# Kernel tuning notes

Hardware: AMD Instinct MI355X
Metric: run time of the kernel (lower is better)

The kernel has to match this reference:

```python
import jax, jax.numpy as jnp
import numpy as np

N = 40000      # nodes
E = 640000     # edges (avg degree 16)
IN = 128
H = 128
OUT = 64


def setup_inputs() -> dict:
    key = jax.random.key(0)
    ks = jax.random.split(key, 10)
    s_in = 1.0 / np.sqrt(IN)
    s_h = 1.0 / np.sqrt(H)
    return {
        "x": jax.random.normal(ks[0], (N, IN), jnp.float32),
        "edge_index": jax.random.randint(ks[1], (2, E), 0, N, dtype=jnp.int64),
        "W1l": jax.random.normal(ks[2], (IN, H), jnp.float32) * s_in,
        "W1r": jax.random.normal(ks[3], (IN, H), jnp.float32) * s_in,
        "b1": jnp.zeros((H,), jnp.float32),
        "W2l": jax.random.normal(ks[4], (H, H), jnp.float32) * s_h,
        "W2r": jax.random.normal(ks[5], (H, H), jnp.float32) * s_h,
        "b2": jnp.zeros((H,), jnp.float32),
        "Wout": jax.random.normal(ks[6], (H, OUT), jnp.float32) * s_h,
        "bout": jnp.zeros((OUT,), jnp.float32),
    }


def _sage_conv(x, src, dst, Wl, Wr, b):
    # mean aggregation of source features onto destination nodes
    msg = x[src]                                   # [E, d] gather
    agg = jax.ops.segment_sum(msg, dst, num_segments=N)       # [N, d]
    deg = jax.ops.segment_sum(jnp.ones((src.shape[0],), x.dtype), dst,
                              num_segments=N)                  # [N]
    agg = agg / jnp.maximum(deg, 1.0)[:, None]
    # PyG SAGEConv: lin_l(aggregated neighbors) + lin_r(root); bias on lin_l
    return agg @ Wl + x @ Wr + b


def reference(x, edge_index, W1l, W1r, b1, W2l, W2r, b2, Wout, bout):
    src, dst = edge_index[0], edge_index[1]
    h = jax.nn.relu(_sage_conv(x, src, dst, W1l, W1r, b1))
    h = jax.nn.relu(_sage_conv(h, src, dst, W2l, W2r, b2))
    return h @ Wout + bout
```

## Files before the change

### kernel.cpp

```cpp
#include <hip/hip_runtime.h>


typedef __attribute__((ext_vector_type(8))) short short8v;
typedef __attribute__((ext_vector_type(4))) float f32x4;
typedef __attribute__((ext_vector_type(4))) _Float16 half4v;
typedef __attribute__((ext_vector_type(8))) _Float16 half8v;

#define CAP 64

static __device__ __forceinline__ unsigned short f2bf(float f) {
  unsigned u = __float_as_uint(f);
  u += 0x7fffu + ((u >> 16) & 1u);
  return (unsigned short)(u >> 16);
}
static __device__ __forceinline__ float bf2f(unsigned short h) {
  return __uint_as_float(((unsigned)h) << 16);
}

__global__ __launch_bounds__(256) void k_setup(
    const int* __restrict__ src, const int* __restrict__ dst,
    int* __restrict__ cnt, ushort* __restrict__ csr,
    const float* __restrict__ W1l, const float* __restrict__ W1r,
    const float* __restrict__ W2l, const float* __restrict__ W2r,
    ushort* __restrict__ w1h, ushort* __restrict__ w1lo,
    ushort* __restrict__ w2h, ushort* __restrict__ w2lo,
    const float* __restrict__ Wout, ushort* __restrict__ woh,
    ushort* __restrict__ wol, const float* __restrict__ x,
    _Float16* __restrict__ xh, int E, int N) {
  int t = blockIdx.x * 256 + threadIdx.x;
  if (t < E) {
    int d = dst[t];
    int pos = atomicAdd(&cnt[d], 1);
    if (pos < CAP) csr[(size_t)d * CAP + pos] = (ushort)src[t];
    return;
  }
  t -= E;
  if (t < 8192) {
    const bool is2 = t >= 4096;
    int u = t & 4095;
    const float* Wl = is2 ? W2l : W1l;
    const float* Wr = is2 ? W2r : W1r;
    ushort* wh = is2 ? w2h : w1h;
    ushort* wlo = is2 ? w2lo : w1lo;
    int l = u & 63;
    int n = (u >> 6) & 7;
    int s = u >> 9;
    int col = n * 16 + (l & 15);
    int kb = s * 32 + ((l >> 4) * 8);
    size_t base = ((size_t)(s * 8 + n) * 64 + l) * 8;
#pragma unroll
    for (int j = 0; j < 8; ++j) {
      int k = kb + j;
      float w = (k < 128) ? Wl[(size_t)k * 128 + col] : Wr[(size_t)(k - 128) * 128 + col];
      unsigned short hb = f2bf(w);
      wh[base + j] = hb;
      wlo[base + j] = f2bf(w - bf2f(hb));
    }
    return;
  }
  t -= 8192;
  if (t < 1024) {
    int l = t & 63;
    int n = (t >> 6) & 3;
    int s = t >> 8;
    int col = n * 16 + (l & 15);
    int kb = s * 32 + ((l >> 4) * 8);
    size_t base = ((size_t)(s * 4 + n) * 64 + l) * 8;
#pragma unroll
    for (int j = 0; j < 8; ++j) {
      float w = Wout[(size_t)(kb + j) * 64 + col];
      unsigned short hb = f2bf(w);
      woh[base + j] = hb;
      wol[base + j] = f2bf(w - bf2f(hb));
    }
    return;
  }
  t -= 1024;
  if (t < N * 32) {
    float4 v = reinterpret_cast<const float4*>(x)[t];
    half4v o = {(_Float16)v.x, (_Float16)v.y, (_Float16)v.z, (_Float16)v.w};
    reinterpret_cast<half4v*>(xh)[t] = o;
  }
}

__global__ __launch_bounds__(256) void k_agg(const _Float16* __restrict__ feat,
                                             const int* __restrict__ cnt,
                                             const ushort* __restrict__ csr,
                                             _Float16* __restrict__ agg, int N) {
  const int lane = threadIdx.x & 63;
  const int q = lane >> 4;
  const int c = (lane & 15) * 8;
  const int wave = threadIdx.x >> 6;
  const int node0 = blockIdx.x * 16 + wave * 4 + q;
  const bool valid = node0 < N;
  const int node = valid ? node0 : (N - 1);
  const int deg = cnt[node];
  const int stored = deg < CAP ? deg : CAP;
  const ushort* idx = csr + (size_t)node * CAP;
  float a[8] = {};
  for (int j = 0; j < stored; j += 8) {
    half8v v0, v1, v2, v3, v4, v5, v6, v7;
    if (j + 0 < stored) { int nb = idx[j + 0]; v0 = *reinterpret_cast<const half8v*>(feat + (size_t)nb * 128 + c); }
    if (j + 1 < stored) { int nb = idx[j + 1]; v1 = *reinterpret_cast<const half8v*>(feat + (size_t)nb * 128 + c); }
    if (j + 2 < stored) { int nb = idx[j + 2]; v2 = *reinterpret_cast<const half8v*>(feat + (size_t)nb * 128 + c); }
    if (j + 3 < stored) { int nb = idx[j + 3]; v3 = *reinterpret_cast<const half8v*>(feat + (size_t)nb * 128 + c); }
    if (j + 4 < stored) { int nb = idx[j + 4]; v4 = *reinterpret_cast<const half8v*>(feat + (size_t)nb * 128 + c); }
    if (j + 5 < stored) { int nb = idx[j + 5]; v5 = *reinterpret_cast<const half8v*>(feat + (size_t)nb * 128 + c); }
    if (j + 6 < stored) { int nb = idx[j + 6]; v6 = *reinterpret_cast<const half8v*>(feat + (size_t)nb * 128 + c); }
    if (j + 7 < stored) { int nb = idx[j + 7]; v7 = *reinterpret_cast<const half8v*>(feat + (size_t)nb * 128 + c); }
#pragma unroll
    for (int t = 0; t < 8; ++t) {
      float s0 = 0.f, s1 = 0.f;
      if (j + 0 < stored) s0 += (float)v0[t];
      if (j + 1 < stored) s1 += (float)v1[t];
      if (j + 2 < stored) s0 += (float)v2[t];
      if (j + 3 < stored) s1 += (float)v3[t];
      if (j + 4 < stored) s0 += (float)v4[t];
      if (j + 5 < stored) s1 += (float)v5[t];
      if (j + 6 < stored) s0 += (float)v6[t];
      if (j + 7 < stored) s1 += (float)v7[t];
      a[t] += s0 + s1;
    }
  }
  if (valid) {
    float invd = 1.0f / fmaxf((float)deg, 1.0f);
    half8v o;
#pragma unroll
    for (int t = 0; t < 8; ++t) o[t] = (_Float16)(a[t] * invd);
    *reinterpret_cast<half8v*>(agg + (size_t)node * 128 + c) = o;
  }
}

__global__ __launch_bounds__(256) void k_gemm1(
    const _Float16* __restrict__ aggh, const _Float16* __restrict__ rooth,
    const ushort* __restrict__ wh, const ushort* __restrict__ wl_,
    const float* __restrict__ bias, _Float16* __restrict__ outh, int M) {
  const int lane = threadIdx.x & 63;
  const int wave = threadIdx.x >> 6;
  const int row = blockIdx.x * 64 + wave * 16;
  f32x4 acc[8] = {};

  for (int s = 0; s < 8; ++s) {
    const int kb = (s & 3) * 32;
    const size_t aoff = (size_t)(row + (lane & 15)) * 128 + kb + (lane >> 4) * 8;
    const _Float16* ap = (s < 4) ? (aggh + aoff) : (rooth + aoff);
    half8v hv = *reinterpret_cast<const half8v*>(ap);
    float av[8];
#pragma unroll
    for (int j = 0; j < 8; ++j) av[j] = (float)hv[j];
    short8v ah, al;
#pragma unroll
    for (int j = 0; j < 8; ++j) {
      unsigned short hb = f2bf(av[j]);
      ah[j] = (short)hb;
      al[j] = (short)f2bf(av[j] - bf2f(hb));
    }
    const size_t sbase = (size_t)s * 8 * 64 * 8 + (size_t)lane * 8;
#pragma unroll
    for (int n = 0; n < 8; ++n) {
      short8v bh = *reinterpret_cast<const short8v*>(wh + sbase + (size_t)n * 64 * 8);
      short8v bl = *reinterpret_cast<const short8v*>(wl_ + sbase + (size_t)n * 64 * 8);
      acc[n] = __builtin_amdgcn_mfma_f32_16x16x32_bf16(ah, bh, acc[n], 0, 0, 0);
      acc[n] = __builtin_amdgcn_mfma_f32_16x16x32_bf16(ah, bl, acc[n], 0, 0, 0);
      acc[n] = __builtin_amdgcn_mfma_f32_16x16x32_bf16(al, bh, acc[n], 0, 0, 0);
    }
  }

  const int r0 = row + (lane >> 4) * 4;
  const int col0 = lane & 15;
#pragma unroll
  for (int n = 0; n < 8; ++n) {
    int col = n * 16 + col0;
    float bv = bias[col];
#pragma unroll
    for (int r = 0; r < 4; ++r) {
      float v = fmaxf(acc[n][r] + bv, 0.f);
      outh[(size_t)(r0 + r) * 128 + col] = (_Float16)v;
    }
  }
}

__global__ __launch_bounds__(256) void k_gemm2_out(
    const _Float16* __restrict__ aggh, const _Float16* __restrict__ rooth,
    const ushort* __restrict__ w2h, const ushort* __restrict__ w2l,
    const float* __restrict__ b2, const ushort* __restrict__ woh,
    const ushort* __restrict__ wol, const float* __restrict__ bout,
    float* __restrict__ out, int M) {
  __shared__ float H[64][132];
  const int lane = threadIdx.x & 63;
  const int wave = threadIdx.x >> 6;
  const int row = blockIdx.x * 64 + wave * 16;
  f32x4 acc[8] = {};

  for (int s = 0; s < 8; ++s) {
    const int kb = (s & 3) * 32;
    const size_t aoff = (size_t)(row + (lane & 15)) * 128 + kb + (lane >> 4) * 8;
    const _Float16* ap = (s < 4) ? (aggh + aoff) : (rooth + aoff);
    half8v hv = *reinterpret_cast<const half8v*>(ap);
    float av[8];
#pragma unroll
    for (int j = 0; j < 8; ++j) av[j] = (float)hv[j];
    short8v ah, al;
#pragma unroll
    for (int j = 0; j < 8; ++j) {
      unsigned short hb = f2bf(av[j]);
      ah[j] = (short)hb;
      al[j] = (short)f2bf(av[j] - bf2f(hb));
    }
    const size_t sbase = (size_t)s * 8 * 64 * 8 + (size_t)lane * 8;
#pragma unroll
    for (int n = 0; n < 8; ++n) {
      short8v bh = *reinterpret_cast<const short8v*>(w2h + sbase + (size_t)n * 64 * 8);
      short8v bl = *reinterpret_cast<const short8v*>(w2l + sbase + (size_t)n * 64 * 8);
      acc[n] = __builtin_amdgcn_mfma_f32_16x16x32_bf16(ah, bh, acc[n], 0, 0, 0);
      acc[n] = __builtin_amdgcn_mfma_f32_16x16x32_bf16(ah, bl, acc[n], 0, 0, 0);
      acc[n] = __builtin_amdgcn_mfma_f32_16x16x32_bf16(al, bh, acc[n], 0, 0, 0);
    }
  }

  const int r0loc = wave * 16 + (lane >> 4) * 4;
  const int col0 = lane & 15;
#pragma unroll
  for (int n = 0; n < 8; ++n) {
    int col = n * 16 + col0;
    float bv = b2[col];
#pragma unroll
    for (int r = 0; r < 4; ++r) {
      H[r0loc + r][col] = fmaxf(acc[n][r] + bv, 0.f);
    }
  }
  __syncthreads();

  f32x4 acc2[4] = {};
  for (int s = 0; s < 4; ++s) {
    const float* hp = &H[wave * 16 + (lane & 15)][s * 32 + (lane >> 4) * 8];
    float av[8];
#pragma unroll
    for (int j = 0; j < 8; ++j) av[j] = hp[j];
    short8v ah, al;
#pragma unroll
    for (int j = 0; j < 8; ++j) {
      unsigned short hb = f2bf(av[j]);
      ah[j] = (short)hb;
      al[j] = (short)f2bf(av[j] - bf2f(hb));
    }
    const size_t sbase = (size_t)s * 4 * 64 * 8 + (size_t)lane * 8;
#pragma unroll
    for (int n = 0; n < 4; ++n) {
      short8v bh = *reinterpret_cast<const short8v*>(woh + sbase + (size_t)n * 64 * 8);
      short8v bl = *reinterpret_cast<const short8v*>(wol + sbase + (size_t)n * 64 * 8);
      acc2[n] = __builtin_amdgcn_mfma_f32_16x16x32_bf16(ah, bh, acc2[n], 0, 0, 0);
      acc2[n] = __builtin_amdgcn_mfma_f32_16x16x32_bf16(ah, bl, acc2[n], 0, 0, 0);
      acc2[n] = __builtin_amdgcn_mfma_f32_16x16x32_bf16(al, bh, acc2[n], 0, 0, 0);
    }
  }

  const int r0 = row + (lane >> 4) * 4;
#pragma unroll
  for (int n = 0; n < 4; ++n) {
    int col = n * 16 + col0;
    float bv = bout[col];
#pragma unroll
    for (int r = 0; r < 4; ++r) {
      out[(size_t)(r0 + r) * 64 + col] = acc2[n][r] + bv;
    }
  }
}

extern "C" void kernel_launch(void* const* d_in, const int* in_sizes, int n_in,
                              void* d_out, int out_size, void* d_ws, size_t ws_size,
                              hipStream_t stream) {
  const float* x    = (const float*)d_in[0];
  const int*   ei   = (const int*)d_in[1];
  const float* W1l  = (const float*)d_in[2];
  const float* W1r  = (const float*)d_in[3];
  const float* b1   = (const float*)d_in[4];
  const float* W2l  = (const float*)d_in[5];
  const float* W2r  = (const float*)d_in[6];
  const float* b2   = (const float*)d_in[7];
  const float* Wout = (const float*)d_in[8];
  const float* bout = (const float*)d_in[9];
  float* out = (float*)d_out;

  const int N = in_sizes[0] / 128;
  const int E = in_sizes[1] / 2;
  const int* src = ei;
  const int* dst = ei + E;

  auto align = [](size_t b) { return (b + 255) & ~(size_t)255; };
  char* p = (char*)d_ws;
  int* cnt       = (int*)p;       p += align((size_t)N * 4);
  ushort* csr    = (ushort*)p;    p += align((size_t)N * CAP * 2);
  _Float16* xh   = (_Float16*)p;  p += align((size_t)N * 128 * 2);
  _Float16* h1h  = (_Float16*)p;  p += align((size_t)N * 128 * 2);
  _Float16* aggh = (_Float16*)p;  p += align((size_t)N * 128 * 2);
  ushort* w1h    = (ushort*)p;    p += align(32768 * 2);
  ushort* w1lo   = (ushort*)p;    p += align(32768 * 2);
  ushort* w2h    = (ushort*)p;    p += align(32768 * 2);
  ushort* w2lo   = (ushort*)p;    p += align(32768 * 2);
  ushort* woh    = (ushort*)p;    p += align(8192 * 2);
  ushort* wol    = (ushort*)p;    p += align(8192 * 2);

  (void)hipMemsetAsync(cnt, 0, (size_t)N * 4, stream);

  const int gemmBlocks = (N + 63) / 64;
  const int aggBlocks = (N + 15) / 16;
  const int setupThreads = E + 8192 + 1024 + N * 32;

  k_setup<<<(setupThreads + 255) / 256, 256, 0, stream>>>(
      src, dst, cnt, csr, W1l, W1r, W2l, W2r, w1h, w1lo, w2h, w2lo,
      Wout, woh, wol, x, xh, E, N);

  k_agg<<<aggBlocks, 256, 0, stream>>>(xh, cnt, csr, aggh, N);
  k_gemm1<<<gemmBlocks, 256, 0, stream>>>(aggh, xh, w1h, w1lo, b1, h1h, N);

  k_agg<<<aggBlocks, 256, 0, stream>>>(h1h, cnt, csr, aggh, N);
  k_gemm2_out<<<gemmBlocks, 256, 0, stream>>>(aggh, h1h, w2h, w2lo, b2,
                                              woh, wol, bout, out, N);
}
```

Before: 148.4 us.

## Fuse neighbor aggregation into GEMM kernels via shared-memory tile

Merges the separate aggregation kernel into each layer's GEMM kernel. Each 64-row block gathers and averages its neighbors into an LDS tile, then feeds the MFMA loop from LDS instead of a global agg buffer. This removes the agg buffer's write and read round trip and two kernel launches. In exchange, each block runs the latency-bound gather (4 passes per wave) before its GEMM, with fewer blocks and extra LDS, which may lower occupancy and the latency hiding of the gather. The validity guard for partial tiles is dropped, which relies on N being a multiple of 64 (40000 is).

Measured after the change: 160.5 us. 1.08x slower.

```diff
diff --git a/kernel.cpp b/kernel.cpp
--- a/kernel.cpp
+++ b/kernel.cpp
@@ -83,71 +83,81 @@
   }
 }
 
-__global__ __launch_bounds__(256) void k_agg(const _Float16* __restrict__ feat,
-                                             const int* __restrict__ cnt,
-                                             const ushort* __restrict__ csr,
-                                             _Float16* __restrict__ agg, int N) {
+static __device__ __forceinline__ void gather_tile(
+    const _Float16* __restrict__ feat, const int* __restrict__ cnt,
+    const ushort* __restrict__ csr, _Float16 (*aggL)[136], int m0) {
   const int lane = threadIdx.x & 63;
   const int q = lane >> 4;
   const int c = (lane & 15) * 8;
   const int wave = threadIdx.x >> 6;
-  const int node0 = blockIdx.x * 16 + wave * 4 + q;
-  const bool valid = node0 < N;
-  const int node = valid ? node0 : (N - 1);
-  const int deg = cnt[node];
-  const int stored = deg < CAP ? deg : CAP;
-  const ushort* idx = csr + (size_t)node * CAP;
-  float a[8] = {};
-  for (int j = 0; j < stored; j += 8) {
-    half8v v0, v1, v2, v3, v4, v5, v6, v7;
-    if (j + 0 < stored) { int nb = idx[j + 0]; v0 = *reinterpret_cast<const half8v*>(feat + (size_t)nb * 128 + c); }
-    if (j + 1 < stored) { int nb = idx[j + 1]; v1 = *reinterpret_cast<const half8v*>(feat + (size_t)nb * 128 + c); }
-    if (j + 2 < stored) { int nb = idx[j + 2]; v2 = *reinterpret_cast<const half8v*>(feat + (size_t)nb * 128 + c); }
-    if (j + 3 < stored) { int nb = idx[j + 3]; v3 = *reinterpret_cast<const half8v*>(feat + (size_t)nb * 128 + c); }
-    if (j + 4 < stored) { int nb = idx[j + 4]; v4 = *reinterpret_cast<const half8v*>(feat + (size_t)nb * 128 + c); }
-    if (j + 5 < stored) { int nb = idx[j + 5]; v5 = *reinterpret_cast<const half8v*>(feat + (size_t)nb * 128 + c); }
-    if (j + 6 < stored) { int nb = idx[j + 6]; v6 = *reinterpret_cast<const half8v*>(feat + (size_t)nb * 128 + c); }
-    if (j + 7 < stored) { int nb = idx[j + 7]; v7 = *reinterpret_cast<const half8v*>(feat + (size_t)nb * 128 + c); }
-#pragma unroll
-    for (int t = 0; t < 8; ++t) {
-      float s0 = 0.f, s1 = 0.f;
-      if (j + 0 < stored) s0 += (float)v0[t];
-      if (j + 1 < stored) s1 += (float)v1[t];
-      if (j + 2 < stored) s0 += (float)v2[t];
-      if (j + 3 < stored) s1 += (float)v3[t];
-      if (j + 4 < stored) s0 += (float)v4[t];
-      if (j + 5 < stored) s1 += (float)v5[t];
-      if (j + 6 < stored) s0 += (float)v6[t];
-      if (j + 7 < stored) s1 += (float)v7[t];
-      a[t] += s0 + s1;
-    }
-  }
-  if (valid) {
+#pragma unroll
+  for (int pass = 0; pass < 4; ++pass) {
+    const int nl = pass * 16 + wave * 4 + q;
+    const int node = m0 + nl;
+    const int deg = cnt[node];
+    const int stored = deg < CAP ? deg : CAP;
+    const ushort* idx = csr + (size_t)node * CAP;
+    float a[8] = {};
+    for (int j = 0; j < stored; j += 8) {
+      half8v v0, v1, v2, v3, v4, v5, v6, v7;
+      if (j + 0 < stored) { int nb = idx[j + 0]; v0 = *reinterpret_cast<const half8v*>(feat + (size_t)nb * 128 + c); }
+      if (j + 1 < stored) { int nb = idx[j + 1]; v1 = *reinterpret_cast<const half8v*>(feat + (size_t)nb * 128 + c); }
+      if (j + 2 < stored) { int nb = idx[j + 2]; v2 = *reinterpret_cast<const half8v*>(feat + (size_t)nb * 128 + c); }
+      if (j + 3 < stored) { int nb = idx[j + 3]; v3 = *reinterpret_cast<const half8v*>(feat + (size_t)nb * 128 + c); }
+      if (j + 4 < stored) { int nb = idx[j + 4]; v4 = *reinterpret_cast<const half8v*>(feat + (size_t)nb * 128 + c); }
+      if (j + 5 < stored) { int nb = idx[j + 5]; v5 = *reinterpret_cast<const half8v*>(feat + (size_t)nb * 128 + c); }
+      if (j + 6 < stored) { int nb = idx[j + 6]; v6 = *reinterpret_cast<const half8v*>(feat + (size_t)nb * 128 + c); }
+      if (j + 7 < stored) { int nb = idx[j + 7]; v7 = *reinterpret_cast<const half8v*>(feat + (size_t)nb * 128 + c); }
+#pragma unroll
+      for (int t = 0; t < 8; ++t) {
+        float s0 = 0.f, s1 = 0.f;
+        if (j + 0 < stored) s0 += (float)v0[t];
+        if (j + 1 < stored) s1 += (float)v1[t];
+        if (j + 2 < stored) s0 += (float)v2[t];
+        if (j + 3 < stored) s1 += (float)v3[t];
+        if (j + 4 < stored) s0 += (float)v4[t];
+        if (j + 5 < stored) s1 += (float)v5[t];
+        if (j + 6 < stored) s0 += (float)v6[t];
+        if (j + 7 < stored) s1 += (float)v7[t];
+        a[t] += s0 + s1;
+      }
+    }
     float invd = 1.0f / fmaxf((float)deg, 1.0f);
     half8v o;
 #pragma unroll
     for (int t = 0; t < 8; ++t) o[t] = (_Float16)(a[t] * invd);
-    *reinterpret_cast<half8v*>(agg + (size_t)node * 128 + c) = o;
-  }
-}
-
-__global__ __launch_bounds__(256) void k_gemm1(
-    const _Float16* __restrict__ aggh, const _Float16* __restrict__ rooth,
-    const ushort* __restrict__ wh, const ushort* __restrict__ wl_,
-    const float* __restrict__ bias, _Float16* __restrict__ outh, int M) {
+    *reinterpret_cast<half8v*>(&aggL[nl][c]) = o;
+  }
+}
+
+__global__ __launch_bounds__(256) void k_fused1(
+    const _Float16* __restrict__ xh, const int* __restrict__ cnt,
+    const ushort* __restrict__ csr, const ushort* __restrict__ wh,
+    const ushort* __restrict__ wl_, const float* __restrict__ bias,
+    _Float16* __restrict__ outh, int M) {
+  __shared__ _Float16 aggL[64][136];
   const int lane = threadIdx.x & 63;
   const int wave = threadIdx.x >> 6;
-  const int row = blockIdx.x * 64 + wave * 16;
+  const int m0 = blockIdx.x * 64;
+  gather_tile(xh, cnt, csr, aggL, m0);
+  __syncthreads();
+
+  const int row = m0 + wave * 16;
   f32x4 acc[8] = {};
-
   for (int s = 0; s < 8; ++s) {
     const int kb = (s & 3) * 32;
-    const size_t aoff = (size_t)(row + (lane & 15)) * 128 + kb + (lane >> 4) * 8;
-    const _Float16* ap = (s < 4) ? (aggh + aoff) : (rooth + aoff);
-    half8v hv = *reinterpret_cast<const half8v*>(ap);
     float av[8];
-#pragma unroll
-    for (int j = 0; j < 8; ++j) av[j] = (float)hv[j];
+    if (s < 4) {
+      const _Float16* lp = &aggL[wave * 16 + (lane & 15)][kb + (lane >> 4) * 8];
+      half8v hv = *reinterpret_cast<const half8v*>(lp);
+#pragma unroll
+      for (int j = 0; j < 8; ++j) av[j] = (float)hv[j];
+    } else {
+      const size_t aoff = (size_t)(row + (lane & 15)) * 128 + kb + (lane >> 4) * 8;
+      half8v hv = *reinterpret_cast<const half8v*>(xh + aoff);
+#pragma unroll
+      for (int j = 0; j < 8; ++j) av[j] = (float)hv[j];
+    }
     short8v ah, al;
 #pragma unroll
     for (int j = 0; j < 8; ++j) {
@@ -180,26 +190,36 @@
   }
 }
 
-__global__ __launch_bounds__(256) void k_gemm2_out(
-    const _Float16* __restrict__ aggh, const _Float16* __restrict__ rooth,
-    const ushort* __restrict__ w2h, const ushort* __restrict__ w2l,
-    const float* __restrict__ b2, const ushort* __restrict__ woh,
-    const ushort* __restrict__ wol, const float* __restrict__ bout,
-    float* __restrict__ out, int M) {
+__global__ __launch_bounds__(256) void k_fused2(
+    const _Float16* __restrict__ h1h, const int* __restrict__ cnt,
+    const ushort* __restrict__ csr, const ushort* __restrict__ w2h,
+    const ushort* __restrict__ w2l, const float* __restrict__ b2,
+    const ushort* __restrict__ woh, const ushort* __restrict__ wol,
+    const float* __restrict__ bout, float* __restrict__ out, int M) {
+  __shared__ _Float16 aggL[64][136];
   __shared__ float H[64][132];
   const int lane = threadIdx.x & 63;
   const int wave = threadIdx.x >> 6;
-  const int row = blockIdx.x * 64 + wave * 16;
+  const int m0 = blockIdx.x * 64;
+  gather_tile(h1h, cnt, csr, aggL, m0);
+  __syncthreads();
+
+  const int row = m0 + wave * 16;
   f32x4 acc[8] = {};
-
   for (int s = 0; s < 8; ++s) {
     const int kb = (s & 3) * 32;
-    const size_t aoff = (size_t)(row + (lane & 15)) * 128 + kb + (lane >> 4) * 8;
-    const _Float16* ap = (s < 4) ? (aggh + aoff) : (rooth + aoff);
-    half8v hv = *reinterpret_cast<const half8v*>(ap);
     float av[8];
-#pragma unroll
-    for (int j = 0; j < 8; ++j) av[j] = (float)hv[j];
+    if (s < 4) {
+      const _Float16* lp = &aggL[wave * 16 + (lane & 15)][kb + (lane >> 4) * 8];
+      half8v hv = *reinterpret_cast<const half8v*>(lp);
+#pragma unroll
+      for (int j = 0; j < 8; ++j) av[j] = (float)hv[j];
+    } else {
+      const size_t aoff = (size_t)(row + (lane & 15)) * 128 + kb + (lane >> 4) * 8;
+      half8v hv = *reinterpret_cast<const half8v*>(h1h + aoff);
+#pragma unroll
+      for (int j = 0; j < 8; ++j) av[j] = (float)hv[j];
+    }
     short8v ah, al;
 #pragma unroll
     for (int j = 0; j < 8; ++j) {
@@ -289,32 +309,28 @@
 
   auto align = [](size_t b) { return (b + 255) & ~(size_t)255; };
   char* p = (char*)d_ws;
-  int* cnt       = (int*)p;       p += align((size_t)N * 4);
-  ushort* csr    = (ushort*)p;    p += align((size_t)N * CAP * 2);
-  _Float16* xh   = (_Float16*)p;  p += align((size_t)N * 128 * 2);
-  _Float16* h1h  = (_Float16*)p;  p += align((size_t)N * 128 * 2);
-  _Float16* aggh = (_Float16*)p;  p += align((size_t)N * 128 * 2);
-  ushort* w1h    = (ushort*)p;    p += align(32768 * 2);
-  ushort* w1lo   = (ushort*)p;    p += align(32768 * 2);
-  ushort* w2h    = (ushort*)p;    p += align(32768 * 2);
-  ushort* w2lo   = (ushort*)p;    p += align(32768 * 2);
-  ushort* woh    = (ushort*)p;    p += align(8192 * 2);
-  ushort* wol    = (ushort*)p;    p += align(8192 * 2);
+  int* cnt      = (int*)p;       p += align((size_t)N * 4);
+  ushort* csr   = (ushort*)p;    p += align((size_t)N * CAP * 2);
+  _Float16* xh  = (_Float16*)p;  p += align((size_t)N * 128 * 2);
+  _Float16* h1h = (_Float16*)p;  p += align((size_t)N * 128 * 2);
+  ushort* w1h   = (ushort*)p;    p += align(32768 * 2);
+  ushort* w1lo  = (ushort*)p;    p += align(32768 * 2);
+  ushort* w2h   = (ushort*)p;    p += align(32768 * 2);
+  ushort* w2lo  = (ushort*)p;    p += align(32768 * 2);
+  ushort* woh   = (ushort*)p;    p += align(8192 * 2);
+  ushort* wol   = (ushort*)p;    p += align(8192 * 2);
 
   (void)hipMemsetAsync(cnt, 0, (size_t)N * 4, stream);
 
   const int gemmBlocks = (N + 63) / 64;
-  const int aggBlocks = (N + 15) / 16;
   const int setupThreads = E + 8192 + 1024 + N * 32;
 
   k_setup<<<(setupThreads + 255) / 256, 256, 0, stream>>>(
       src, dst, cnt, csr, W1l, W1r, W2l, W2r, w1h, w1lo, w2h, w2lo,
       Wout, woh, wol, x, xh, E, N);
 
-  k_agg<<<aggBlocks, 256, 0, stream>>>(xh, cnt, csr, aggh, N);
-  k_gemm1<<<gemmBlocks, 256, 0, stream>>>(aggh, xh, w1h, w1lo, b1, h1h, N);
-
-  k_agg<<<aggBlocks, 256, 0, stream>>>(h1h, cnt, csr, aggh, N);
-  k_gemm2_out<<<gemmBlocks, 256, 0, stream>>>(aggh, h1h, w2h, w2lo, b2,
-                                              woh, wol, bout, out, N);
-}
+  k_fused1<<<gemmBlocks, 256, 0, stream>>>(xh, cnt, csr, w1h, w1lo, b1, h1h, N);
+
+  k_fused2<<<gemmBlocks, 256, 0, stream>>>(h1h, cnt, csr, w2h, w2lo, b2,
+                                           woh, wol, bout, out, N);
+}
```
